# Kernel tuning notes

Measured on AMD Instinct MI355X. Metric: run time of the kernel, lower is better.

## Reference

```python
import jax, jax.numpy as jnp
import numpy as np

N_VERTS = 100000
N_FACES = 200000
C = 512


def setup_inputs() -> dict:
    key = jax.random.key(0)
    ks = jax.random.split(key, 12)
    x = jax.random.normal(ks[0], (1, N_VERTS, C), dtype=jnp.float32) * 0.1
    verts = jax.random.normal(ks[1], (N_VERTS, 3), dtype=jnp.float32)
    faces = jax.random.randint(ks[2], (N_FACES, 3), 0, N_VERTS, dtype=jnp.int32)
    def lin(k, fan_in, fan_out):
        return jax.random.normal(k, (fan_in, fan_out), dtype=jnp.float32) / np.sqrt(fan_in)
    return {
        "x": x, "verts": verts, "faces": faces,
        "W1": lin(ks[3], C, C),    "b1": jnp.zeros((C,), jnp.float32),
        "W2": lin(ks[4], C, 512),  "b2": jnp.zeros((512,), jnp.float32),
        "W3": lin(ks[5], 512, 256),"b3": jnp.zeros((256,), jnp.float32),
        "W4": lin(ks[6], 256, 12), "b4": jnp.zeros((12,), jnp.float32),
    }


def special_procrustes(M):
    # roma.special_procrustes: nearest rotation in SO(3) to M, batched [F,3,3]
    U, S, Vh = jnp.linalg.svd(M)
    det = jnp.linalg.det(jnp.matmul(U, Vh))  # [F]
    D = jnp.stack([jnp.ones_like(det), jnp.ones_like(det), det], axis=-1)  # [F,3]
    return jnp.matmul(U * D[:, None, :], Vh)


def reference(x, verts, faces, W1, b1, W2, b2, W3, b3, W4, b4):
    N = verts.shape[0]
    F = faces.shape[0]
    # prism base: gather 3 vertex positions per face -> [F,3,3]
    prism_base = verts[faces]
    # gather features of the 3 face vertices and mean over them -> [F,C]
    feat = x[0][faces].mean(axis=1)
    # mlp_refine
    h = jax.nn.relu(feat @ W1 + b1)
    h = jax.nn.relu(h @ W2 + b2)
    h = jax.nn.relu(h @ W3 + b3)
    out = h @ W4 + b4  # [F,12]
    # batched 3x3 Procrustes rotation + translation
    rotations = special_procrustes(out[:, :9].reshape(F, 3, 3))
    translations = out[:, 9:]  # [F,3]
    transformed_prism = jnp.matmul(prism_base, rotations) + translations[:, None, :]  # [F,3,3]
    # scatter-add back to vertices with per-vertex face-count normalization
    flat_idx = faces.reshape(-1)  # [3F]
    summed = jax.ops.segment_sum(transformed_prism.reshape(-1, 3), flat_idx, num_segments=N)
    counts = jax.ops.segment_sum(jnp.ones((3 * F,), jnp.float32), flat_idx, num_segments=N)
    features = summed / jnp.clip(counts, 1.0)[:, None]  # [N,3]
    return features[None], transformed_prism, rotations
```

## Files before the change

kernel.cpp:

```cpp
#include <hip/hip_runtime.h>
#include <stdint.h>

typedef __attribute__((ext_vector_type(8))) short short8;
typedef __attribute__((ext_vector_type(4))) float f32x4;
typedef __attribute__((ext_vector_type(4))) unsigned short u16x4;

__device__ __forceinline__ unsigned short f2bf(float x) {
    union { float f; uint32_t u; } v; v.f = x;
    uint32_t u = v.u;
    uint32_t r = (u + 0x7FFFu + ((u >> 16) & 1u)) >> 16;
    return (unsigned short)r;
}
__device__ __forceinline__ float bf2f(unsigned short h) {
    union { uint32_t u; float f; } v; v.u = ((uint32_t)h) << 16;
    return v.f;
}
__device__ __forceinline__ void splitT(float f, unsigned short& hi, unsigned short& lo) {
    union { float f; uint32_t u; } a; a.f = f;
    hi = (unsigned short)(a.u >> 16);
    union { uint32_t u; float f; } b; b.u = a.u & 0xFFFF0000u;
    union { float f; uint32_t u; } c; c.f = f - b.f;
    lo = (unsigned short)(c.u >> 16);
}

__device__ __forceinline__ void gld_lds16(const void* g, void* s) {
    __builtin_amdgcn_global_load_lds(
        (const __attribute__((address_space(1))) void*)(uintptr_t)g,
        (__attribute__((address_space(3))) void*)(uint32_t)(uintptr_t)s,
        16, 0, 0);
}

__device__ __forceinline__ f32x4 mfma16(short8 a, short8 b, f32x4 c) {
    return __builtin_amdgcn_mfma_f32_16x16x32_bf16(a, b, c, 0, 0, 0);
}

__global__ void zero_kernel(float* __restrict__ sums, float* __restrict__ counts, int nverts) {
    int t = blockIdx.x * 256 + threadIdx.x;
    if (t < nverts * 3) sums[t] = 0.0f;
    if (t < nverts)     counts[t] = 0.0f;
}

__global__ void prep_weights(const float* __restrict__ W1, const float* __restrict__ W2,
                             const float* __restrict__ W3,
                             unsigned short* __restrict__ w1h, unsigned short* __restrict__ w1l,
                             unsigned short* __restrict__ w2h, unsigned short* __restrict__ w2l,
                             unsigned short* __restrict__ w3h, unsigned short* __restrict__ w3l) {
    int t = blockIdx.x * 256 + threadIdx.x;
    float v; unsigned short *ph, *pl; size_t o;
    if (t < 262144) {
        int k = t >> 9, n = t & 511;
        v = W1[t]; o = (size_t)n * 512 + k; ph = w1h; pl = w1l;
    } else if (t < 524288) {
        int u = t - 262144; int k = u >> 9, n = u & 511;
        v = W2[u]; o = (size_t)n * 512 + k; ph = w2h; pl = w2l;
    } else if (t < 655360) {
        int u = t - 524288; int k = u >> 8, n = u & 255;
        v = W3[u]; o = (size_t)n * 512 + k; ph = w3h; pl = w3l;
    } else return;
    unsigned short hi = f2bf(v);
    unsigned short lo = f2bf(v - bf2f(hi));
    ph[o] = hi; pl[o] = lo;
}

__global__ void gather_mean(const float* __restrict__ x, const int* __restrict__ faces,
                            unsigned short* __restrict__ Fhi, unsigned short* __restrict__ Flo,
                            int fbase, int fcount, int mrows) {
    int t = blockIdx.x * 256 + threadIdx.x;
    if (t >= (mrows << 7)) return;
    int r = t >> 7;
    int c = (t & 127) << 2;
    f32x4 m = {0.f, 0.f, 0.f, 0.f};
    if (r < fcount) {
        int f = fbase + r;
        int i0 = faces[3 * f], i1 = faces[3 * f + 1], i2 = faces[3 * f + 2];
        f32x4 a = *(const f32x4*)(x + (size_t)i0 * 512 + c);
        f32x4 b = *(const f32x4*)(x + (size_t)i1 * 512 + c);
        f32x4 d = *(const f32x4*)(x + (size_t)i2 * 512 + c);
        m = (a + b + d) * (1.0f / 3.0f);
    }
    u16x4 hv, lv;
#pragma unroll
    for (int j = 0; j < 4; ++j) {
        unsigned short hi = f2bf(m[j]);
        hv[j] = hi;
        lv[j] = f2bf(m[j] - bf2f(hi));
    }
    *(u16x4*)(Fhi + (size_t)r * 512 + c) = hv;
    *(u16x4*)(Flo + (size_t)r * 512 + c) = lv;
}

template<int OUT>
__global__ __launch_bounds__(256, 2)
void gemm_pipe(const unsigned short* __restrict__ Ahi, const unsigned short* __restrict__ Alo,
               const unsigned short* __restrict__ Bhi, const unsigned short* __restrict__ Blo,
               const float* __restrict__ bias,
               void* __restrict__ Out0, unsigned short* __restrict__ Olo,
               int N, int K, int nt) {
    __shared__ __align__(16) unsigned short sm[2][4][128 * 32];

    const int tid  = threadIdx.x;
    const int lane = tid & 63;
    const int w    = tid >> 6;
    const int wr = w >> 1, wc = w & 1;

    const int nwg  = gridDim.x;
    const int orig = blockIdx.x;
    const int q = nwg >> 3, r8 = nwg & 7;
    const int xcd = orig & 7, idx = orig >> 3;
    const int wg = (xcd < r8 ? xcd * (q + 1) : r8 * (q + 1) + (xcd - r8) * q) + idx;
    const int m0 = (wg / nt) << 7;
    const int n0 = (wg % nt) << 7;

    f32x4 acc[4][4] = {};

    const int s_lo  = w * 64 + lane;
    const int row0  = s_lo >> 2;
    const int c0    = ((s_lo & 3) - ((row0 >> 1) & 3)) & 3;
    const int s_hi  = 256 + s_lo;
    const int row1  = (s_hi >> 2) & 127;
    const int c1    = ((s_hi & 3) - ((row1 >> 1) & 3)) & 3;

    auto stage = [&](int b, int t) {
        const int k0 = t << 5;
        const unsigned short* const mats[4] = {Ahi, Alo, Bhi, Blo};
#pragma unroll
        for (int p = 0; p < 4; ++p) {
            const unsigned short* mat = mats[p];
            const int base0 = (p < 2) ? m0 : n0;
            gld_lds16(mat + (size_t)(base0 + row0) * K + (k0 + (c0 << 3)),
                      &sm[b][p][(w * 64) * 8]);
            gld_lds16(mat + (size_t)(base0 + row1) * K + (k0 + (c1 << 3)),
                      &sm[b][p][(256 + w * 64) * 8]);
        }
    };

    const int NT = K >> 5;
    stage(0, 0);
    stage(1, 1);

    const int kc  = lane >> 4;
    const int rbA = (wr << 6) + (lane & 15);
    const int rbB = (wc << 6) + (lane & 15);

    for (int t = 0; t < NT; ++t) {
        const int cur = t & 1;

        if (t + 1 < NT) asm volatile("s_waitcnt vmcnt(8)" ::: "memory");
        else            asm volatile("s_waitcnt vmcnt(0)" ::: "memory");
        __builtin_amdgcn_s_barrier();

        short8 ah[4], al[4], bh[4], bl[4];
#pragma unroll
        for (int m = 0; m < 4; ++m) {
            const int r   = rbA + (m << 4);
            const int off = r * 32 + (((kc + (r >> 1)) & 3) << 3);
            ah[m] = *(const short8*)&sm[cur][0][off];
            al[m] = *(const short8*)&sm[cur][1][off];
        }
#pragma unroll
        for (int n = 0; n < 4; ++n) {
            const int r   = rbB + (n << 4);
            const int off = r * 32 + (((kc + (r >> 1)) & 3) << 3);
            bh[n] = *(const short8*)&sm[cur][2][off];
            bl[n] = *(const short8*)&sm[cur][3][off];
        }
        asm volatile("s_waitcnt lgkmcnt(0)" ::: "memory");
        __builtin_amdgcn_sched_barrier(0);
        __builtin_amdgcn_s_barrier();

        if (t + 2 < NT) stage(cur, t + 2);

        __builtin_amdgcn_s_setprio(1);
#pragma unroll
        for (int m = 0; m < 4; ++m)
#pragma unroll
            for (int n = 0; n < 4; ++n)
                acc[m][n] = mfma16(ah[m], bh[n], acc[m][n]);
#pragma unroll
        for (int m = 0; m < 4; ++m)
#pragma unroll
            for (int n = 0; n < 4; ++n)
                acc[m][n] = mfma16(al[m], bh[n], acc[m][n]);
#pragma unroll
        for (int m = 0; m < 4; ++m)
#pragma unroll
            for (int n = 0; n < 4; ++n)
                acc[m][n] = mfma16(ah[m], bl[n], acc[m][n]);
        __builtin_amdgcn_s_setprio(0);
    }

#pragma unroll
    for (int n = 0; n < 4; ++n) {
        const int col = n0 + (wc << 6) + (n << 4) + (lane & 15);
        const float bv = (OUT == 1) ? 0.0f : bias[col];
#pragma unroll
        for (int m = 0; m < 4; ++m) {
            const int rbase = m0 + (wr << 6) + (m << 4) + ((lane >> 4) << 2);
#pragma unroll
            for (int j = 0; j < 4; ++j) {
                const size_t o = (size_t)(rbase + j) * N + col;
                if (OUT == 1) {
                    ((float*)Out0)[o] = acc[m][n][j];
                } else if (OUT == 2) {
                    ((float*)Out0)[o] = fmaxf(acc[m][n][j] + bv, 0.0f);
                } else {
                    float v = fmaxf(acc[m][n][j] + bv, 0.0f);
                    unsigned short hi = f2bf(v);
                    ((unsigned short*)Out0)[o] = hi;
                    Olo[o] = f2bf(v - bf2f(hi));
                }
            }
        }
    }
}

__global__ __launch_bounds__(256, 2)
void gemm_l1(const float* __restrict__ X,
             const unsigned short* __restrict__ Bhi, const unsigned short* __restrict__ Blo,
             float* __restrict__ Out,
             int N, int K, int nt, int nvalid) {
    __shared__ __align__(16) unsigned short sm[2][4][128 * 32];

    const int tid  = threadIdx.x;
    const int lane = tid & 63;
    const int w    = tid >> 6;
    const int wr = w >> 1, wc = w & 1;

    const int nwg  = gridDim.x;
    const int orig = blockIdx.x;
    const int q = nwg >> 3, r8 = nwg & 7;
    const int xcd = orig & 7, idx = orig >> 3;
    const int wg = (xcd < r8 ? xcd * (q + 1) : r8 * (q + 1) + (xcd - r8) * q) + idx;
    const int m0 = (wg / nt) << 7;
    const int n0 = (wg % nt) << 7;

    f32x4 acc[4][4] = {};

    int arow[2], achk[2], adst[2], avalid[2];
#pragma unroll
    for (int i = 0; i < 2; ++i) {
        const int s   = i * 256 + tid;
        const int row = s >> 2;
        const int c   = s & 3;
        arow[i]   = row;
        achk[i]   = c;
        adst[i]   = row * 32 + (((c + (row >> 1)) & 3) << 3);
        avalid[i] = (m0 + row) < nvalid;
    }
    const int s_lo  = w * 64 + lane;
    const int row0  = s_lo >> 2;
    const int c0    = ((s_lo & 3) - ((row0 >> 1) & 3)) & 3;
    const int s_hi  = 256 + s_lo;
    const int row1  = (s_hi >> 2) & 127;
    const int c1    = ((s_hi & 3) - ((row1 >> 1) & 3)) & 3;

    f32x4 fA[2][2];

    auto issueA = [&](int t) {
        const int k0 = t << 5;
#pragma unroll
        for (int i = 0; i < 2; ++i) {
            const int gr = avalid[i] ? (m0 + arow[i]) : 0;
            const float* src = X + (size_t)gr * K + (k0 + (achk[i] << 3));
            fA[i][0] = *(const f32x4*)src;
            fA[i][1] = *(const f32x4*)(src + 4);
        }
    };
    auto issueB = [&](int b, int t) {
        const int k0 = t << 5;
        gld_lds16(Bhi + (size_t)(n0 + row0) * K + (k0 + (c0 << 3)), &sm[b][2][(w * 64) * 8]);
        gld_lds16(Bhi + (size_t)(n0 + row1) * K + (k0 + (c1 << 3)), &sm[b][2][(256 + w * 64) * 8]);
        gld_lds16(Blo + (size_t)(n0 + row0) * K + (k0 + (c0 << 3)), &sm[b][3][(w * 64) * 8]);
        gld_lds16(Blo + (size_t)(n0 + row1) * K + (k0 + (c1 << 3)), &sm[b][3][(256 + w * 64) * 8]);
    };
    auto cvtWriteA = [&](int b) {
#pragma unroll
        for (int i = 0; i < 2; ++i) {
            short8 hv, lv;
#pragma unroll
            for (int j = 0; j < 8; ++j) {
                float f = avalid[i] ? fA[i][j >> 2][j & 3] : 0.0f;
                unsigned short hi, lo;
                splitT(f, hi, lo);
                hv[j] = (short)hi;
                lv[j] = (short)lo;
            }
            *(short8*)&sm[b][0][adst[i]] = hv;
            *(short8*)&sm[b][1][adst[i]] = lv;
        }
    };

    const int NT = K >> 5;
    issueA(0); issueB(0, 0);
    asm volatile("s_waitcnt vmcnt(4)" ::: "memory");
    cvtWriteA(0);
    issueA(1); issueB(1, 1);
    asm volatile("s_waitcnt vmcnt(4)" ::: "memory");
    cvtWriteA(1);
    asm volatile("s_waitcnt lgkmcnt(0)" ::: "memory");

    const int kc  = lane >> 4;
    const int rbA = (wr << 6) + (lane & 15);
    const int rbB = (wc << 6) + (lane & 15);

    for (int t = 0; t < NT; ++t) {
        const int cur = t & 1;

        if (t + 1 < NT) asm volatile("s_waitcnt vmcnt(4)" ::: "memory");
        else            asm volatile("s_waitcnt vmcnt(0)" ::: "memory");
        __builtin_amdgcn_s_barrier();

        short8 ah[4], al[4], bh[4], bl[4];
#pragma unroll
        for (int m = 0; m < 4; ++m) {
            const int r   = rbA + (m << 4);
            const int off = r * 32 + (((kc + (r >> 1)) & 3) << 3);
            ah[m] = *(const short8*)&sm[cur][0][off];
            al[m] = *(const short8*)&sm[cur][1][off];
        }
#pragma unroll
        for (int n = 0; n < 4; ++n) {
            const int r   = rbB + (n << 4);
            const int off = r * 32 + (((kc + (r >> 1)) & 3) << 3);
            bh[n] = *(const short8*)&sm[cur][2][off];
            bl[n] = *(const short8*)&sm[cur][3][off];
        }
        asm volatile("s_waitcnt lgkmcnt(0)" ::: "memory");
        __builtin_amdgcn_sched_barrier(0);
        __builtin_amdgcn_s_barrier();

        const int doStage = (t + 2 < NT);
        if (doStage) { issueA(t + 2); issueB(cur, t + 2); }

        __builtin_amdgcn_s_setprio(1);
#pragma unroll
        for (int m = 0; m < 4; ++m)
#pragma unroll
            for (int n = 0; n < 4; ++n)
                acc[m][n] = mfma16(ah[m], bh[n], acc[m][n]);
#pragma unroll
        for (int m = 0; m < 4; ++m)
#pragma unroll
            for (int n = 0; n < 4; ++n)
                acc[m][n] = mfma16(al[m], bh[n], acc[m][n]);
#pragma unroll
        for (int m = 0; m < 4; ++m)
#pragma unroll
            for (int n = 0; n < 4; ++n)
                acc[m][n] = mfma16(ah[m], bl[n], acc[m][n]);
        __builtin_amdgcn_s_setprio(0);

        if (doStage) {
            asm volatile("s_waitcnt vmcnt(4)" ::: "memory");
            cvtWriteA(cur);
        }
    }

#pragma unroll
    for (int n = 0; n < 4; ++n) {
        const int col = n0 + (wc << 6) + (n << 4) + (lane & 15);
#pragma unroll
        for (int m = 0; m < 4; ++m) {
            const int rbase = m0 + (wr << 6) + (m << 4) + ((lane >> 4) << 2);
#pragma unroll
            for (int j = 0; j < 4; ++j)
                Out[(size_t)(rbase + j) * N + col] = acc[m][n][j];
        }
    }
}

__global__ __launch_bounds__(256, 2)
void gemm_l2g(const float* __restrict__ Y, const int* __restrict__ faces,
              const float* __restrict__ b1,
              const unsigned short* __restrict__ Bhi, const unsigned short* __restrict__ Blo,
              const float* __restrict__ bias2,
              unsigned short* __restrict__ Ohi, unsigned short* __restrict__ Olo,
              int N, int K, int nt, int nvalid) {
    __shared__ __align__(16) unsigned short sm[2][4][128 * 32];

    const int tid  = threadIdx.x;
    const int lane = tid & 63;
    const int w    = tid >> 6;
    const int wr = w >> 1, wc = w & 1;

    const int nwg  = gridDim.x;
    const int orig = blockIdx.x;
    const int q = nwg >> 3, r8 = nwg & 7;
    const int xcd = orig & 7, idx = orig >> 3;
    const int wg = (xcd < r8 ? xcd * (q + 1) : r8 * (q + 1) + (xcd - r8) * q) + idx;
    const int m0 = (wg / nt) << 7;
    const int n0 = (wg % nt) << 7;

    f32x4 acc[4][4] = {};

    int adst[2], avalid[2];
    int fidx[2][3];
    const int achk = tid & 3;
#pragma unroll
    for (int i = 0; i < 2; ++i) {
        const int s   = i * 256 + tid;
        const int row = s >> 2;
        adst[i]   = row * 32 + (((achk + (row >> 1)) & 3) << 3);
        const int gf  = m0 + row;
        avalid[i] = gf < nvalid;
        const int gfs = avalid[i] ? gf : 0;
        fidx[i][0] = faces[3 * gfs];
        fidx[i][1] = faces[3 * gfs + 1];
        fidx[i][2] = faces[3 * gfs + 2];
    }
    const int s_lo  = w * 64 + lane;
    const int row0  = s_lo >> 2;
    const int c0    = ((s_lo & 3) - ((row0 >> 1) & 3)) & 3;
    const int s_hi  = 256 + s_lo;
    const int row1  = (s_hi >> 2) & 127;
    const int c1    = ((s_hi & 3) - ((row1 >> 1) & 3)) & 3;

    f32x4 fA[2][3][2];
    f32x4 fb[2];

    auto issueA = [&](int t) {
        const int koff = (t << 5) + (achk << 3);
#pragma unroll
        for (int i = 0; i < 2; ++i) {
#pragma unroll
            for (int r = 0; r < 3; ++r) {
                const float* src = Y + (size_t)fidx[i][r] * K + koff;
                fA[i][r][0] = *(const f32x4*)src;
                fA[i][r][1] = *(const f32x4*)(src + 4);
            }
        }
        fb[0] = *(const f32x4*)(b1 + koff);
        fb[1] = *(const f32x4*)(b1 + koff + 4);
    };
    auto issueB = [&](int b, int t) {
        const int k0 = t << 5;
        gld_lds16(Bhi + (size_t)(n0 + row0) * K + (k0 + (c0 << 3)), &sm[b][2][(w * 64) * 8]);
        gld_lds16(Bhi + (size_t)(n0 + row1) * K + (k0 + (c1 << 3)), &sm[b][2][(256 + w * 64) * 8]);
        gld_lds16(Blo + (size_t)(n0 + row0) * K + (k0 + (c0 << 3)), &sm[b][3][(w * 64) * 8]);
        gld_lds16(Blo + (size_t)(n0 + row1) * K + (k0 + (c1 << 3)), &sm[b][3][(256 + w * 64) * 8]);
    };
    auto cvtWriteA = [&](int b) {
        const float third = 1.0f / 3.0f;
#pragma unroll
        for (int i = 0; i < 2; ++i) {
            short8 hv, lv;
#pragma unroll
            for (int j = 0; j < 8; ++j) {
                const int h = j >> 2, e = j & 3;
                float f = 0.0f;
                if (avalid[i]) {
                    f = (fA[i][0][h][e] + fA[i][1][h][e] + fA[i][2][h][e]) * third + fb[h][e];
                    f = fmaxf(f, 0.0f);
                }
                unsigned short hi, lo;
                splitT(f, hi, lo);
                hv[j] = (short)hi;
                lv[j] = (short)lo;
            }
            *(short8*)&sm[b][0][adst[i]] = hv;
            *(short8*)&sm[b][1][adst[i]] = lv;
        }
    };

    const int NT = K >> 5;
    issueA(0); issueB(0, 0);
    asm volatile("s_waitcnt vmcnt(4)" ::: "memory");
    cvtWriteA(0);
    issueA(1); issueB(1, 1);
    asm volatile("s_waitcnt vmcnt(4)" ::: "memory");
    cvtWriteA(1);
    asm volatile("s_waitcnt lgkmcnt(0)" ::: "memory");

    const int kc  = lane >> 4;
    const int rbA = (wr << 6) + (lane & 15);
    const int rbB = (wc << 6) + (lane & 15);

    for (int t = 0; t < NT; ++t) {
        const int cur = t & 1;

        if (t + 1 < NT) asm volatile("s_waitcnt vmcnt(4)" ::: "memory");
        else            asm volatile("s_waitcnt vmcnt(0)" ::: "memory");
        __builtin_amdgcn_s_barrier();

        if (t + 2 < NT) issueA(t + 2);

        short8 ah[4], al[4], bh[4], bl[4];
#pragma unroll
        for (int m = 0; m < 4; ++m) {
            const int r   = rbA + (m << 4);
            const int off = r * 32 + (((kc + (r >> 1)) & 3) << 3);
            ah[m] = *(const short8*)&sm[cur][0][off];
            al[m] = *(const short8*)&sm[cur][1][off];
        }
#pragma unroll
        for (int n = 0; n < 4; ++n) {
            const int r   = rbB + (n << 4);
            const int off = r * 32 + (((kc + (r >> 1)) & 3) << 3);
            bh[n] = *(const short8*)&sm[cur][2][off];
            bl[n] = *(const short8*)&sm[cur][3][off];
        }
        asm volatile("s_waitcnt lgkmcnt(0)" ::: "memory");
        __builtin_amdgcn_sched_barrier(0);
        __builtin_amdgcn_s_barrier();

        if (t + 2 < NT) issueB(cur, t + 2);

        __builtin_amdgcn_s_setprio(1);
#pragma unroll
        for (int m = 0; m < 4; ++m)
#pragma unroll
            for (int n = 0; n < 4; ++n)
                acc[m][n] = mfma16(ah[m], bh[n], acc[m][n]);
#pragma unroll
        for (int m = 0; m < 4; ++m)
#pragma unroll
            for (int n = 0; n < 4; ++n)
                acc[m][n] = mfma16(al[m], bh[n], acc[m][n]);
#pragma unroll
        for (int m = 0; m < 4; ++m)
#pragma unroll
            for (int n = 0; n < 4; ++n)
                acc[m][n] = mfma16(ah[m], bl[n], acc[m][n]);
        __builtin_amdgcn_s_setprio(0);

        if (t + 2 < NT) {
            asm volatile("s_waitcnt vmcnt(4)" ::: "memory");
            cvtWriteA(cur);
        }
    }

#pragma unroll
    for (int n = 0; n < 4; ++n) {
        const int col = n0 + (wc << 6) + (n << 4) + (lane & 15);
        const float bv = bias2[col];
#pragma unroll
        for (int m = 0; m < 4; ++m) {
            const int rbase = m0 + (wr << 6) + (m << 4) + ((lane >> 4) << 2);
#pragma unroll
            for (int j = 0; j < 4; ++j) {
                const size_t o = (size_t)(rbase + j) * N + col;
                float v = fmaxf(acc[m][n][j] + bv, 0.0f);
                unsigned short hi, lo;
                splitT(v, hi, lo);
                Ohi[o] = hi;
                Olo[o] = lo;
            }
        }
    }
}

#define JROT(app, aqq, apq, apz, aqz, vp0, vp1, vp2, vq0, vq1, vq2) do {          \
    float _apq = (apq);                                                            \
    if (fabsf(_apq) > 1e-30f) {                                                    \
        float _tau = ((aqq) - (app)) / (2.0f * _apq);                              \
        float _t = copysignf(1.0f, _tau) / (fabsf(_tau) + sqrtf(1.0f + _tau*_tau));\
        float _c = 1.0f / sqrtf(1.0f + _t*_t);                                     \
        float _s = _t * _c;                                                        \
        (app) = (app) - _t * _apq;                                                 \
        (aqq) = (aqq) + _t * _apq;                                                 \
        (apq) = 0.0f;                                                              \
        float _pz = (apz), _qz = (aqz);                                            \
        (apz) = _c * _pz - _s * _qz;                                               \
        (aqz) = _s * _pz + _c * _qz;                                               \
        float _x;                                                                  \
        _x = (vp0); (vp0) = _c*_x - _s*(vq0); (vq0) = _s*_x + _c*(vq0);            \
        _x = (vp1); (vp1) = _c*_x - _s*(vq1); (vq1) = _s*_x + _c*(vq1);            \
        _x = (vp2); (vp2) = _c*_x - _s*(vq2); (vq2) = _s*_x + _c*(vq2);            \
    }                                                                              \
} while (0)

#define SWAP3(la, lb, x0, y0, z0, x1, y1, z1) do {                \
    float _tm;                                                    \
    _tm = la; la = lb; lb = _tm;                                  \
    _tm = x0; x0 = x1; x1 = _tm;                                  \
    _tm = y0; y0 = y1; y1 = _tm;                                  \
    _tm = z0; z0 = z1; z1 = _tm;                                  \
} while (0)

__global__ void face_kernel(const float* __restrict__ H3,
                            const float* __restrict__ W4, const float* __restrict__ b4,
                            const float* __restrict__ verts, const int* __restrict__ faces,
                            float* __restrict__ out_tp, float* __restrict__ out_rot,
                            float* __restrict__ sums, float* __restrict__ counts,
                            int fbase, int fcount) {
    __shared__ float sW[256 * 12 + 12];
    for (int i = threadIdx.x; i < 256 * 12 + 12; i += 256)
        sW[i] = (i < 256 * 12) ? W4[i] : b4[i - 256 * 12];
    __syncthreads();

    const int r = blockIdx.x * 256 + threadIdx.x;
    if (r >= fcount) return;
    const int f = fbase + r;

    float o[12];
#pragma unroll
    for (int n = 0; n < 12; ++n) o[n] = sW[3072 + n];
    const f32x4* ph = (const f32x4*)(H3 + (size_t)r * 256);
    for (int kb = 0; kb < 64; ++kb) {
        f32x4 hv = ph[kb];
#pragma unroll
        for (int kk = 0; kk < 4; ++kk) {
            float val = hv[kk];
            const float* wrow = &sW[(kb * 4 + kk) * 12];
#pragma unroll
            for (int n = 0; n < 12; ++n) o[n] = fmaf(val, wrow[n], o[n]);
        }
    }

    const float M00=o[0], M01=o[1], M02=o[2];
    const float M10=o[3], M11=o[4], M12=o[5];
    const float M20=o[6], M21=o[7], M22=o[8];
    const float t0 =o[9], t1 =o[10], t2 =o[11];

    float a00 = M00*M00 + M10*M10 + M20*M20;
    float a11 = M01*M01 + M11*M11 + M21*M21;
    float a22 = M02*M02 + M12*M12 + M22*M22;
    float a01 = M00*M01 + M10*M11 + M20*M21;
    float a02 = M00*M02 + M10*M12 + M20*M22;
    float a12 = M01*M02 + M11*M12 + M21*M22;

    float v00=1.f, v01=0.f, v02=0.f;
    float v10=0.f, v11=1.f, v12=0.f;
    float v20=0.f, v21=0.f, v22=1.f;
#pragma unroll
    for (int sweep = 0; sweep < 5; ++sweep) {
        JROT(a00, a11, a01, a02, a12, v00, v10, v20, v01, v11, v21);
        JROT(a00, a22, a02, a01, a12, v00, v10, v20, v02, v12, v22);
        JROT(a11, a22, a12, a01, a02, v01, v11, v21, v02, v12, v22);
    }
    float l0 = a00, l1 = a11, l2 = a22;
    if (l0 < l1) SWAP3(l0, l1, v00, v10, v20, v01, v11, v21);
    if (l0 < l2) SWAP3(l0, l2, v00, v10, v20, v02, v12, v22);
    if (l1 < l2) SWAP3(l1, l2, v01, v11, v21, v02, v12, v22);

    float b1x = M00*v00 + M01*v10 + M02*v20;
    float b1y = M10*v00 + M11*v10 + M12*v20;
    float b1z = M20*v00 + M21*v10 + M22*v20;
    float b2x = M00*v01 + M01*v11 + M02*v21;
    float b2y = M10*v01 + M11*v11 + M12*v21;
    float b2z = M20*v01 + M21*v11 + M22*v21;

    float n1 = sqrtf(b1x*b1x + b1y*b1y + b1z*b1z);
    float u1x, u1y, u1z;
    if (n1 > 1e-25f) { float in = 1.0f / n1; u1x = b1x*in; u1y = b1y*in; u1z = b1z*in; }
    else             { u1x = 1.f; u1y = 0.f; u1z = 0.f; }

    float dp  = b2x*u1x + b2y*u1y + b2z*u1z;
    float w2x = b2x - dp*u1x, w2y = b2y - dp*u1y, w2z = b2z - dp*u1z;
    float n2  = sqrtf(w2x*w2x + w2y*w2y + w2z*w2z);
    float u2x, u2y, u2z;
    if (n2 > 1e-25f) { float in = 1.0f / n2; u2x = w2x*in; u2y = w2y*in; u2z = w2z*in; }
    else {
        float ex = (fabsf(u1x) < 0.9f) ? 1.f : 0.f;
        float ey = 1.f - ex;
        float cx = -u1z * ey, cy = u1z * ex, cz = u1x * ey - u1y * ex;
        float cn = rsqrtf(cx*cx + cy*cy + cz*cz);
        u2x = cx * cn; u2y = cy * cn; u2z = cz * cn;
    }
    float u3x = u1y*u2z - u1z*u2y;
    float u3y = u1z*u2x - u1x*u2z;
    float u3z = u1x*u2y - u1y*u2x;

    float dv = v00*(v11*v22 - v12*v21) - v01*(v10*v22 - v12*v20) + v02*(v10*v21 - v11*v20);
    if (dv < 0.f) { v02 = -v02; v12 = -v12; v22 = -v22; }

    float R00 = u1x*v00 + u2x*v01 + u3x*v02;
    float R01 = u1x*v10 + u2x*v11 + u3x*v12;
    float R02 = u1x*v20 + u2x*v21 + u3x*v22;
    float R10 = u1y*v00 + u2y*v01 + u3y*v02;
    float R11 = u1y*v10 + u2y*v11 + u3y*v12;
    float R12 = u1y*v20 + u2y*v21 + u3y*v22;
    float R20 = u1z*v00 + u2z*v01 + u3z*v02;
    float R21 = u1z*v10 + u2z*v11 + u3z*v12;
    float R22 = u1z*v20 + u2z*v21 + u3z*v22;

    float* rp = out_rot + (size_t)f * 9;
    rp[0]=R00; rp[1]=R01; rp[2]=R02;
    rp[3]=R10; rp[4]=R11; rp[5]=R12;
    rp[6]=R20; rp[7]=R21; rp[8]=R22;

    float* tp = out_tp + (size_t)f * 9;
    const int idx[3] = { faces[3*f], faces[3*f+1], faces[3*f+2] };
#pragma unroll
    for (int j = 0; j < 3; ++j) {
        const int vi = idx[j];
        float px = verts[3*vi], py = verts[3*vi+1], pz = verts[3*vi+2];
        float q0 = px*R00 + py*R10 + pz*R20 + t0;
        float q1 = px*R01 + py*R11 + pz*R21 + t1;
        float q2 = px*R02 + py*R12 + pz*R22 + t2;
        tp[j*3+0] = q0; tp[j*3+1] = q1; tp[j*3+2] = q2;
        atomicAdd(&sums[(size_t)vi*3+0], q0);
        atomicAdd(&sums[(size_t)vi*3+1], q1);
        atomicAdd(&sums[(size_t)vi*3+2], q2);
        atomicAdd(&counts[vi], 1.0f);
    }
}

__global__ void finalize_kernel(float* __restrict__ feats, const float* __restrict__ counts, int nverts) {
    int v = blockIdx.x * 256 + threadIdx.x;
    if (v >= nverts) return;
    float c = fmaxf(counts[v], 1.0f);
    feats[v*3+0] = feats[v*3+0] / c;
    feats[v*3+1] = feats[v*3+1] / c;
    feats[v*3+2] = feats[v*3+2] / c;
}

extern "C" void kernel_launch(void* const* d_in, const int* in_sizes, int n_in,
                              void* d_out, int out_size, void* d_ws, size_t ws_size,
                              hipStream_t stream) {
    const float* x     = (const float*)d_in[0];
    const float* verts = (const float*)d_in[1];
    const int*   faces = (const int*)d_in[2];
    const float* W1 = (const float*)d_in[3];
    const float* b1 = (const float*)d_in[4];
    const float* W2 = (const float*)d_in[5];
    const float* b2 = (const float*)d_in[6];
    const float* W3 = (const float*)d_in[7];
    const float* b3 = (const float*)d_in[8];
    const float* W4 = (const float*)d_in[9];
    const float* b4 = (const float*)d_in[10];

    const int nverts = in_sizes[1] / 3;
    const int nfaces = in_sizes[2] / 3;

    float* out_feats = (float*)d_out;
    float* out_tp    = out_feats + (size_t)nverts * 3;
    float* out_rot   = out_tp + (size_t)nfaces * 9;

    char* ws = (char*)d_ws;
    size_t cur = 0;
    auto carve = [&](size_t bytes) -> void* {
        void* p = ws + cur;
        cur += (bytes + 255) & ~(size_t)255;
        return p;
    };
    unsigned short* w1h = (unsigned short*)carve(512 * 512 * 2);
    unsigned short* w1l = (unsigned short*)carve(512 * 512 * 2);
    unsigned short* w2h = (unsigned short*)carve(512 * 512 * 2);
    unsigned short* w2l = (unsigned short*)carve(512 * 512 * 2);
    unsigned short* w3h = (unsigned short*)carve(256 * 512 * 2);
    unsigned short* w3l = (unsigned short*)carve(256 * 512 * 2);
    float* counts = (float*)carve((size_t)nverts * 4);

    const long MV = ((long)nverts + 127) & ~127L;
    const long MF = ((long)nfaces + 127) & ~127L;
    const size_t szY   = (size_t)MV * 512 * 4;
    const size_t szH2w = (size_t)MF * 512 * 2;
    const size_t szH3f = (size_t)MF * 256 * 4;

    const size_t sR1 = (szY > szH3f) ? szY : szH3f;
    const size_t sR2 = szH2w;
    const size_t sR3 = szH2w;
    const size_t need = cur + sR1 + sR2 + sR3 + 4 * 256;

    zero_kernel<<<(nverts * 3 + 255) / 256, 256, 0, stream>>>(out_feats, counts, nverts);
    prep_weights<<<(655360 + 255) / 256, 256, 0, stream>>>(W1, W2, W3, w1h, w1l, w2h, w2l, w3h, w3l);

    if (ws_size >= need) {
        char* R1 = (char*)carve(sR1);
        char* R2 = (char*)carve(sR2);
        char* R3 = (char*)carve(sR3);
        float*          y   = (float*)R1;
        float*          h3  = (float*)R1;
        unsigned short* h2h = (unsigned short*)R2;
        unsigned short* h2l = (unsigned short*)R3;

        gemm_l1<<<(int)(MV / 128) * 4, 256, 0, stream>>>(x, w1h, w1l, y, 512, 512, 4, nverts);

        gemm_l2g<<<(int)(MF / 128) * 4, 256, 0, stream>>>(y, faces, b1, w2h, w2l, b2,
                                                          h2h, h2l, 512, 512, 4, nfaces);

        gemm_pipe<2><<<(int)(MF / 128) * 2, 256, 0, stream>>>(h2h, h2l, w3h, w3l, b3, h3, nullptr, 256, 512, 2);

        face_kernel<<<(nfaces + 255) / 256, 256, 0, stream>>>(h3, W4, b4, verts, faces,
                                                              out_tp, out_rot, out_feats, counts,
                                                              0, nfaces);
    } else {
        long mpad = MF;
        size_t avail = (ws_size > cur) ? (ws_size - cur) : 0;
        long chp = (long)(avail / 4096);
        chp &= ~127L;
        if (chp > mpad) chp = mpad;
        if (chp < 128) chp = 128;
        unsigned short* bAh = (unsigned short*)carve((size_t)chp * 512 * 2);
        unsigned short* bAl = (unsigned short*)carve((size_t)chp * 512 * 2);
        unsigned short* bBh = (unsigned short*)carve((size_t)chp * 512 * 2);
        unsigned short* bBl = (unsigned short*)carve((size_t)chp * 512 * 2);

        for (long base = 0; base < nfaces; base += chp) {
            long rem = (long)nfaces - base;
            int cnt = (int)((rem < chp) ? rem : chp);
            int mc  = (cnt + 127) & ~127;

            gather_mean<<<mc / 2, 256, 0, stream>>>(x, faces, bAh, bAl, (int)base, cnt, mc);
            gemm_pipe<0><<<(mc / 128) * 4, 256, 0, stream>>>(bAh, bAl, w1h, w1l, b1, bBh, bBl, 512, 512, 4);
            gemm_pipe<0><<<(mc / 128) * 4, 256, 0, stream>>>(bBh, bBl, w2h, w2l, b2, bAh, bAl, 512, 512, 4);
            gemm_pipe<2><<<(mc / 128) * 2, 256, 0, stream>>>(bAh, bAl, w3h, w3l, b3, (float*)bBh, nullptr, 256, 512, 2);
            face_kernel<<<(cnt + 255) / 256, 256, 0, stream>>>((float*)bBh, W4, b4, verts, faces,
                                                               out_tp, out_rot, out_feats, counts,
                                                               (int)base, cnt);
        }
    }

    finalize_kernel<<<(nverts + 255) / 256, 256, 0, stream>>>(out_feats, counts, nverts);
}
```

Baseline: 1.152 ms.

## Fuse zeroing into weight prep, hoist 32-bit address offsets, switch to RNE split

Merges the zero kernel into prep_weights so one launch goes away. Precomputes per-thread 32-bit base offsets for the GEMM tile loads so the inner loop does less 64-bit address arithmetic. In gemm_l1 the next A-tile global load is issued earlier, right after the barrier, so it overlaps more work. The truncating hi/lo split is replaced with round-to-nearest conversions via hip_bf16 intrinsics, which costs a little more ALU in exchange for better precision. The 32-bit offsets could overflow if sizes grew, since nfaces*512 must fit in uint32.

```diff
diff --git a/kernel.cpp b/kernel.cpp
--- a/kernel.cpp
+++ b/kernel.cpp
@@ -1,4 +1,5 @@
 #include <hip/hip_runtime.h>
+#include <hip/hip_bf16.h>
 #include <stdint.h>
 
 typedef __attribute__((ext_vector_type(8))) short short8;
@@ -15,12 +16,12 @@
     union { uint32_t u; float f; } v; v.u = ((uint32_t)h) << 16;
     return v.f;
 }
-__device__ __forceinline__ void splitT(float f, unsigned short& hi, unsigned short& lo) {
-    union { float f; uint32_t u; } a; a.f = f;
-    hi = (unsigned short)(a.u >> 16);
-    union { uint32_t u; float f; } b; b.u = a.u & 0xFFFF0000u;
-    union { float f; uint32_t u; } c; c.f = f - b.f;
-    lo = (unsigned short)(c.u >> 16);
+__device__ __forceinline__ void split_rne(float f, unsigned short& hi, unsigned short& lo) {
+    __hip_bfloat16 h = __float2bfloat16(f);
+    union { __hip_bfloat16 b; unsigned short u; } ch; ch.b = h; hi = ch.u;
+    float hf = __bfloat162float(h);
+    __hip_bfloat16 l = __float2bfloat16(f - hf);
+    union { __hip_bfloat16 b; unsigned short u; } cl; cl.b = l; lo = cl.u;
 }
 
 __device__ __forceinline__ void gld_lds16(const void* g, void* s) {
@@ -34,18 +35,15 @@
     return __builtin_amdgcn_mfma_f32_16x16x32_bf16(a, b, c, 0, 0, 0);
 }
 
-__global__ void zero_kernel(float* __restrict__ sums, float* __restrict__ counts, int nverts) {
-    int t = blockIdx.x * 256 + threadIdx.x;
-    if (t < nverts * 3) sums[t] = 0.0f;
-    if (t < nverts)     counts[t] = 0.0f;
-}
-
 __global__ void prep_weights(const float* __restrict__ W1, const float* __restrict__ W2,
                              const float* __restrict__ W3,
                              unsigned short* __restrict__ w1h, unsigned short* __restrict__ w1l,
                              unsigned short* __restrict__ w2h, unsigned short* __restrict__ w2l,
-                             unsigned short* __restrict__ w3h, unsigned short* __restrict__ w3l) {
+                             unsigned short* __restrict__ w3h, unsigned short* __restrict__ w3l,
+                             float* __restrict__ sums, float* __restrict__ counts, int nverts) {
     int t = blockIdx.x * 256 + threadIdx.x;
+    if (t < nverts * 3) sums[t] = 0.0f;
+    if (t < nverts)     counts[t] = 0.0f;
     float v; unsigned short *ph, *pl; size_t o;
     if (t < 262144) {
         int k = t >> 9, n = t & 511;
@@ -57,8 +55,8 @@
         int u = t - 524288; int k = u >> 8, n = u & 255;
         v = W3[u]; o = (size_t)n * 512 + k; ph = w3h; pl = w3l;
     } else return;
-    unsigned short hi = f2bf(v);
-    unsigned short lo = f2bf(v - bf2f(hi));
+    unsigned short hi, lo;
+    split_rne(v, hi, lo);
     ph[o] = hi; pl[o] = lo;
 }
 
@@ -81,9 +79,9 @@
     u16x4 hv, lv;
 #pragma unroll
     for (int j = 0; j < 4; ++j) {
-        unsigned short hi = f2bf(m[j]);
-        hv[j] = hi;
-        lv[j] = f2bf(m[j] - bf2f(hi));
+        unsigned short hi, lo;
+        split_rne(m[j], hi, lo);
+        hv[j] = hi; lv[j] = lo;
     }
     *(u16x4*)(Fhi + (size_t)r * 512 + c) = hv;
     *(u16x4*)(Flo + (size_t)r * 512 + c) = lv;
@@ -120,18 +118,21 @@
     const int row1  = (s_hi >> 2) & 127;
     const int c1    = ((s_hi & 3) - ((row1 >> 1) & 3)) & 3;
 
+    const uint32_t oA0 = (uint32_t)(m0 + row0) * (uint32_t)K + (c0 << 3);
+    const uint32_t oA1 = (uint32_t)(m0 + row1) * (uint32_t)K + (c1 << 3);
+    const uint32_t oB0 = (uint32_t)(n0 + row0) * (uint32_t)K + (c0 << 3);
+    const uint32_t oB1 = (uint32_t)(n0 + row1) * (uint32_t)K + (c1 << 3);
+
     auto stage = [&](int b, int t) {
-        const int k0 = t << 5;
-        const unsigned short* const mats[4] = {Ahi, Alo, Bhi, Blo};
-#pragma unroll
-        for (int p = 0; p < 4; ++p) {
-            const unsigned short* mat = mats[p];
-            const int base0 = (p < 2) ? m0 : n0;
-            gld_lds16(mat + (size_t)(base0 + row0) * K + (k0 + (c0 << 3)),
-                      &sm[b][p][(w * 64) * 8]);
-            gld_lds16(mat + (size_t)(base0 + row1) * K + (k0 + (c1 << 3)),
-                      &sm[b][p][(256 + w * 64) * 8]);
-        }
+        const uint32_t k0 = t << 5;
+        gld_lds16(Ahi + oA0 + k0, &sm[b][0][(w * 64) * 8]);
+        gld_lds16(Ahi + oA1 + k0, &sm[b][0][(256 + w * 64) * 8]);
+        gld_lds16(Alo + oA0 + k0, &sm[b][1][(w * 64) * 8]);
+        gld_lds16(Alo + oA1 + k0, &sm[b][1][(256 + w * 64) * 8]);
+        gld_lds16(Bhi + oB0 + k0, &sm[b][2][(w * 64) * 8]);
+        gld_lds16(Bhi + oB1 + k0, &sm[b][2][(256 + w * 64) * 8]);
+        gld_lds16(Blo + oB0 + k0, &sm[b][3][(w * 64) * 8]);
+        gld_lds16(Blo + oB1 + k0, &sm[b][3][(256 + w * 64) * 8]);
     };
 
     const int NT = K >> 5;
@@ -205,9 +206,10 @@
                     ((float*)Out0)[o] = fmaxf(acc[m][n][j] + bv, 0.0f);
                 } else {
                     float v = fmaxf(acc[m][n][j] + bv, 0.0f);
-                    unsigned short hi = f2bf(v);
+                    unsigned short hi, lo;
+                    split_rne(v, hi, lo);
                     ((unsigned short*)Out0)[o] = hi;
-                    Olo[o] = f2bf(v - bf2f(hi));
+                    Olo[o] = lo;
                 }
             }
         }
@@ -236,16 +238,16 @@
 
     f32x4 acc[4][4] = {};
 
-    int arow[2], achk[2], adst[2], avalid[2];
+    int adst[2], avalid[2];
+    uint32_t xoff[2];
 #pragma unroll
     for (int i = 0; i < 2; ++i) {
         const int s   = i * 256 + tid;
         const int row = s >> 2;
         const int c   = s & 3;
-        arow[i]   = row;
-        achk[i]   = c;
         adst[i]   = row * 32 + (((c + (row >> 1)) & 3) << 3);
         avalid[i] = (m0 + row) < nvalid;
+        xoff[i]   = (uint32_t)(avalid[i] ? (m0 + row) : 0) * (uint32_t)K + (c << 3);
     }
     const int s_lo  = w * 64 + lane;
     const int row0  = s_lo >> 2;
@@ -253,25 +255,26 @@
     const int s_hi  = 256 + s_lo;
     const int row1  = (s_hi >> 2) & 127;
     const int c1    = ((s_hi & 3) - ((row1 >> 1) & 3)) & 3;
+    const uint32_t oB0 = (uint32_t)(n0 + row0) * (uint32_t)K + (c0 << 3);
+    const uint32_t oB1 = (uint32_t)(n0 + row1) * (uint32_t)K + (c1 << 3);
 
     f32x4 fA[2][2];
 
     auto issueA = [&](int t) {
-        const int k0 = t << 5;
+        const uint32_t k0 = t << 5;
 #pragma unroll
         for (int i = 0; i < 2; ++i) {
-            const int gr = avalid[i] ? (m0 + arow[i]) : 0;
-            const float* src = X + (size_t)gr * K + (k0 + (achk[i] << 3));
+            const float* src = X + xoff[i] + k0;
             fA[i][0] = *(const f32x4*)src;
             fA[i][1] = *(const f32x4*)(src + 4);
         }
     };
     auto issueB = [&](int b, int t) {
-        const int k0 = t << 5;
-        gld_lds16(Bhi + (size_t)(n0 + row0) * K + (k0 + (c0 << 3)), &sm[b][2][(w * 64) * 8]);
-        gld_lds16(Bhi + (size_t)(n0 + row1) * K + (k0 + (c1 << 3)), &sm[b][2][(256 + w * 64) * 8]);
-        gld_lds16(Blo + (size_t)(n0 + row0) * K + (k0 + (c0 << 3)), &sm[b][3][(w * 64) * 8]);
-        gld_lds16(Blo + (size_t)(n0 + row1) * K + (k0 + (c1 << 3)), &sm[b][3][(256 + w * 64) * 8]);
+        const uint32_t k0 = t << 5;
+        gld_lds16(Bhi + oB0 + k0, &sm[b][2][(w * 64) * 8]);
+        gld_lds16(Bhi + oB1 + k0, &sm[b][2][(256 + w * 64) * 8]);
+        gld_lds16(Blo + oB0 + k0, &sm[b][3][(w * 64) * 8]);
+        gld_lds16(Blo + oB1 + k0, &sm[b][3][(256 + w * 64) * 8]);
     };
     auto cvtWriteA = [&](int b) {
 #pragma unroll
@@ -281,7 +284,7 @@
             for (int j = 0; j < 8; ++j) {
                 float f = avalid[i] ? fA[i][j >> 2][j & 3] : 0.0f;
                 unsigned short hi, lo;
-                splitT(f, hi, lo);
+                split_rne(f, hi, lo);
                 hv[j] = (short)hi;
                 lv[j] = (short)lo;
             }
@@ -310,6 +313,8 @@
         else            asm volatile("s_waitcnt vmcnt(0)" ::: "memory");
         __builtin_amdgcn_s_barrier();
 
+        if (t + 2 < NT) issueA(t + 2);
+
         short8 ah[4], al[4], bh[4], bl[4];
 #pragma unroll
         for (int m = 0; m < 4; ++m) {
@@ -329,8 +334,7 @@
         __builtin_amdgcn_sched_barrier(0);
         __builtin_amdgcn_s_barrier();
 
-        const int doStage = (t + 2 < NT);
-        if (doStage) { issueA(t + 2); issueB(cur, t + 2); }
+        if (t + 2 < NT) issueB(cur, t + 2);
 
         __builtin_amdgcn_s_setprio(1);
 #pragma unroll
@@ -350,7 +354,7 @@
                 acc[m][n] = mfma16(ah[m], bl[n], acc[m][n]);
         __builtin_amdgcn_s_setprio(0);
 
-        if (doStage) {
+        if (t + 2 < NT) {
             asm volatile("s_waitcnt vmcnt(4)" ::: "memory");
             cvtWriteA(cur);
         }
@@ -394,7 +398,7 @@
     f32x4 acc[4][4] = {};
 
     int adst[2], avalid[2];
-    int fidx[2][3];
+    uint32_t yoff[2][3];
     const int achk = tid & 3;
 #pragma unroll
     for (int i = 0; i < 2; ++i) {
@@ -404,9 +408,9 @@
         const int gf  = m0 + row;
         avalid[i] = gf < nvalid;
         const int gfs = avalid[i] ? gf : 0;
-        fidx[i][0] = faces[3 * gfs];
-        fidx[i][1] = faces[3 * gfs + 1];
-        fidx[i][2] = faces[3 * gfs + 2];
+#pragma unroll
+        for (int r = 0; r < 3; ++r)
+            yoff[i][r] = (uint32_t)faces[3 * gfs + r] * (uint32_t)K;
     }
     const int s_lo  = w * 64 + lane;
     const int row0  = s_lo >> 2;
@@ -414,17 +418,19 @@
     const int s_hi  = 256 + s_lo;
     const int row1  = (s_hi >> 2) & 127;
     const int c1    = ((s_hi & 3) - ((row1 >> 1) & 3)) & 3;
+    const uint32_t oB0 = (uint32_t)(n0 + row0) * (uint32_t)K + (c0 << 3);
+    const uint32_t oB1 = (uint32_t)(n0 + row1) * (uint32_t)K + (c1 << 3);
 
     f32x4 fA[2][3][2];
     f32x4 fb[2];
 
     auto issueA = [&](int t) {
-        const int koff = (t << 5) + (achk << 3);
+        const uint32_t koff = (uint32_t)(t << 5) + (achk << 3);
 #pragma unroll
         for (int i = 0; i < 2; ++i) {
 #pragma unroll
             for (int r = 0; r < 3; ++r) {
-                const float* src = Y + (size_t)fidx[i][r] * K + koff;
+                const float* src = Y + yoff[i][r] + koff;
                 fA[i][r][0] = *(const f32x4*)src;
                 fA[i][r][1] = *(const f32x4*)(src + 4);
             }
@@ -433,11 +439,11 @@
         fb[1] = *(const f32x4*)(b1 + koff + 4);
     };
     auto issueB = [&](int b, int t) {
-        const int k0 = t << 5;
-        gld_lds16(Bhi + (size_t)(n0 + row0) * K + (k0 + (c0 << 3)), &sm[b][2][(w * 64) * 8]);
-        gld_lds16(Bhi + (size_t)(n0 + row1) * K + (k0 + (c1 << 3)), &sm[b][2][(256 + w * 64) * 8]);
-        gld_lds16(Blo + (size_t)(n0 + row0) * K + (k0 + (c0 << 3)), &sm[b][3][(w * 64) * 8]);
-        gld_lds16(Blo + (size_t)(n0 + row1) * K + (k0 + (c1 << 3)), &sm[b][3][(256 + w * 64) * 8]);
+        const uint32_t k0 = t << 5;
+        gld_lds16(Bhi + oB0 + k0, &sm[b][2][(w * 64) * 8]);
+        gld_lds16(Bhi + oB1 + k0, &sm[b][2][(256 + w * 64) * 8]);
+        gld_lds16(Blo + oB0 + k0, &sm[b][3][(w * 64) * 8]);
+        gld_lds16(Blo + oB1 + k0, &sm[b][3][(256 + w * 64) * 8]);
     };
     auto cvtWriteA = [&](int b) {
         const float third = 1.0f / 3.0f;
@@ -449,11 +455,11 @@
                 const int h = j >> 2, e = j & 3;
                 float f = 0.0f;
                 if (avalid[i]) {
-                    f = (fA[i][0][h][e] + fA[i][1][h][e] + fA[i][2][h][e]) * third + fb[h][e];
+                    f = fmaf(fA[i][0][h][e] + fA[i][1][h][e] + fA[i][2][h][e], third, fb[h][e]);
                     f = fmaxf(f, 0.0f);
                 }
                 unsigned short hi, lo;
-                splitT(f, hi, lo);
+                split_rne(f, hi, lo);
                 hv[j] = (short)hi;
                 lv[j] = (short)lo;
             }
@@ -541,7 +547,7 @@
                 const size_t o = (size_t)(rbase + j) * N + col;
                 float v = fmaxf(acc[m][n][j] + bv, 0.0f);
                 unsigned short hi, lo;
-                splitT(v, hi, lo);
+                split_rne(v, hi, lo);
                 Ohi[o] = hi;
                 Olo[o] = lo;
             }
@@ -753,8 +759,8 @@
     const size_t sR3 = szH2w;
     const size_t need = cur + sR1 + sR2 + sR3 + 4 * 256;
 
-    zero_kernel<<<(nverts * 3 + 255) / 256, 256, 0, stream>>>(out_feats, counts, nverts);
-    prep_weights<<<(655360 + 255) / 256, 256, 0, stream>>>(W1, W2, W3, w1h, w1l, w2h, w2l, w3h, w3l);
+    prep_weights<<<(655360 + 255) / 256, 256, 0, stream>>>(W1, W2, W3, w1h, w1l, w2h, w2l, w3h, w3l,
+                                                           out_feats, counts, nverts);
 
     if (ws_size >= need) {
         char* R1 = (char*)carve(sR1);
```

Result: no change. 1.156 ms (+0.3%).
